# Optimization experiments

Measured on AMD Instinct MI355X. Metric: run time of the kernel, lower is better.

## Reference

```python
import jax, jax.numpy as jnp
import numpy as np
from jax import lax

EPS = 1e-5

def conv2d(x, w, b, pad):
    y = lax.conv_general_dilated(x, w, (1, 1), [(pad, pad), (pad, pad)],
                                 dimension_numbers=('NCHW', 'OIHW', 'NCHW'))
    return y + b[None, :, None, None]

def batchnorm(x, gamma, beta):
    mean = jnp.mean(x, axis=(0, 2, 3), keepdims=True)
    var = jnp.var(x, axis=(0, 2, 3), keepdims=True)  # biased, as torch BN training mode
    return gamma[None, :, None, None] * (x - mean) * lax.rsqrt(var + EPS) + beta[None, :, None, None]

def maxpool2(x):
    return lax.reduce_window(x, -jnp.inf, lax.max, (1, 1, 2, 2), (1, 1, 2, 2), 'VALID')

def upsample(x, s):
    N, C, H, W = x.shape
    return jax.image.resize(x, (N, C, H * s, W * s), method='bilinear')

def select_topvar(x, k=3):
    # per-sample, per-channel unbiased variance; gather top-k variance channels
    N, C, H, W = x.shape
    v = jnp.var(x.reshape(N, C, H * W), axis=-1, ddof=1)  # [N, C]
    _, idx = lax.top_k(v, k)                              # argsort(-v)[:k]
    return jnp.take_along_axis(x, idx[:, :, None, None], axis=1)

def setup_inputs() -> dict:
    key = jax.random.key(0)
    ks = jax.random.split(key, 16)
    n_channel, n_class = 10, 5
    d = {}
    d['x'] = jax.random.normal(ks[0], (16, n_channel, 512, 512), jnp.float32)
    sc = 0.1
    d['w_ext1'] = jax.random.normal(ks[1], (16, n_channel, 1, 1), jnp.float32) * sc
    d['b_ext1'] = jnp.zeros((16,), jnp.float32)
    d['g_ebn1'] = jnp.ones((16,), jnp.float32)
    d['be_ebn1'] = jnp.zeros((16,), jnp.float32)
    d['w_ext2'] = jax.random.normal(ks[2], (16, 16, 1, 1), jnp.float32) * sc
    d['b_ext2'] = jnp.zeros((16,), jnp.float32)
    d['g_ebn2'] = jnp.ones((16,), jnp.float32)
    d['be_ebn2'] = jnp.zeros((16,), jnp.float32)
    d['w_c1'] = jax.random.normal(ks[3], (8, 3, 3, 3), jnp.float32) * sc
    d['b_c1'] = jnp.zeros((8,), jnp.float32)
    d['w_c2'] = jax.random.normal(ks[4], (16, 8, 3, 3), jnp.float32) * sc
    d['b_c2'] = jnp.zeros((16,), jnp.float32)
    d['g_bn1'] = jnp.ones((16,), jnp.float32)
    d['be_bn1'] = jnp.zeros((16,), jnp.float32)
    d['g_bn2'] = jnp.ones((8,), jnp.float32)
    d['be_bn2'] = jnp.zeros((8,), jnp.float32)
    d['w_1k'] = jax.random.normal(ks[5], (n_class, 24, 1, 1), jnp.float32) * sc
    d['b_1k'] = jnp.zeros((n_class,), jnp.float32)
    return d

def reference(x, w_ext1, b_ext1, g_ebn1, be_ebn1, w_ext2, b_ext2, g_ebn2, be_ebn2,
              w_c1, b_c1, w_c2, b_c2, g_bn1, be_bn1, g_bn2, be_bn2, w_1k, b_1k):
    # bandExtract: 1x1 conv -> BN -> sigmoid, twice
    h = jax.nn.sigmoid(batchnorm(conv2d(x, w_ext1, b_ext1, 0), g_ebn1, be_ebn1))
    h = jax.nn.sigmoid(batchnorm(conv2d(h, w_ext2, b_ext2, 0), g_ebn2, be_ebn2))
    # featureSelect: keep 3 channels with largest per-sample variance
    x0 = select_topvar(h, 3)                                   # [N,3,H,W]
    x1 = maxpool2(jax.nn.sigmoid(conv2d(x0, w_c1, b_c1, 1)))   # [N,8,H/2,W/2]
    x2 = maxpool2(jax.nn.sigmoid(conv2d(x1, w_c2, b_c2, 1)))   # [N,16,H/4,W/4]
    x2 = batchnorm(jax.nn.relu(upsample(x2, 4)), g_bn1, be_bn1)  # [N,16,H,W]
    x1 = batchnorm(jax.nn.relu(upsample(x1, 2)), g_bn2, be_bn2)  # [N,8,H,W]
    merge = jnp.concatenate([x1, x2], axis=1)                    # [N,24,H,W]
    return conv2d(merge, w_1k, b_1k, 0)                          # [N,n_class,H,W]
```

## Files before the change

### kernel.cpp

```cpp
#include <hip/hip_runtime.h>
#include <hip/hip_fp16.h>
#include <math.h>

#define N_    16
#define CIN_  10
#define CB_   16
#define H_    512
#define W_    512
#define HW_   (512*512)
#define EPSF  1e-5f

__device__ __forceinline__ float sgm(float z){
  float e = __builtin_amdgcn_exp2f(z * -1.44269504088896f);
  return __builtin_amdgcn_rcpf(1.0f + e);
}

__global__ void k_zero(double* __restrict__ p, int n){
  int i = blockIdx.x*256 + threadIdx.x;
  if (i < n) p[i] = 0.0;
}

template<int NB, int C>
__global__ void k_finp(const double* __restrict__ P, const float* __restrict__ g,
                       const float* __restrict__ be, float* __restrict__ AB, double invM){
  __shared__ double rs[256], rq[256];
  const int t = threadIdx.x;
  const int c = t % C, slot = t / C, nslot = 256 / C;
  const int tot = N_ * NB;
  double s=0.0, q=0.0;
  for (int j = slot; j < tot; j += nslot){
    int n = j / NB, b = j - n*NB;
    size_t idx = ((size_t)((n*C + c)*NB + b))*2;
    s += P[idx]; q += P[idx+1];
  }
  rs[t]=s; rq[t]=q; __syncthreads();
  for (int h = nslot>>1; h>0; h>>=1){
    if (slot < h){ rs[t] += rs[t + h*C]; rq[t] += rq[t + h*C]; }
    __syncthreads();
  }
  if (slot == 0){
    double mean = rs[c]*invM;
    double var  = rq[c]*invM - mean*mean;
    float a = g[c]*rsqrtf((float)var + EPSF);
    AB[c]   = a;
    AB[C+c] = be[c] - (float)mean*a;
  }
}

__global__ void k_fin2(const double* __restrict__ S1, const float* __restrict__ g1,
                       const float* __restrict__ be1, float* __restrict__ A1,
                       const double* __restrict__ S2, const float* __restrict__ g2,
                       const float* __restrict__ be2, float* __restrict__ A2,
                       double invM){
  const double* S = (blockIdx.x==0) ? S1 : S2;
  const float*  g = (blockIdx.x==0) ? g1 : g2;
  const float* be = (blockIdx.x==0) ? be1 : be2;
  float*       AB = (blockIdx.x==0) ? A1 : A2;
  const int     C = (blockIdx.x==0) ? 16 : 8;
  int c = threadIdx.x;
  if (c < C){
    double s=0.0,q=0.0;
    for (int n=0;n<N_;++n){ s+=S[(n*C+c)*2]; q+=S[(n*C+c)*2+1]; }
    double mean = s*invM;
    double var  = q*invM - mean*mean;
    float a = g[c]*rsqrtf((float)var + EPSF);
    AB[c]   = a;
    AB[C+c] = be[c] - (float)mean*a;
  }
}

__global__ __launch_bounds__(256) void k_cov(
    const float* __restrict__ x, double* __restrict__ SP)
{
  const int n = blockIdx.y;
  const int base = blockIdx.x*4096;
  const float* xp = x + (size_t)n*CIN_*HW_;
  float s[CIN_], p[55];
#pragma unroll
  for (int i=0;i<CIN_;++i) s[i]=0.f;
#pragma unroll
  for (int i=0;i<55;++i) p[i]=0.f;
#pragma unroll 1
  for (int it=0; it<4; ++it){
    const int off = base + it*1024 + threadIdx.x*4;
    float4 xv[CIN_];
#pragma unroll
    for (int ci=0; ci<CIN_; ++ci)
      xv[ci] = *(const float4*)(xp + (size_t)ci*HW_ + off);
#pragma unroll
    for (int ci=0; ci<CIN_; ++ci)
      s[ci] += xv[ci].x + xv[ci].y + xv[ci].z + xv[ci].w;
    int k=0;
#pragma unroll
    for (int i=0;i<CIN_;++i)
#pragma unroll
      for (int j=i;j<CIN_;++j,++k)
        p[k] += xv[i].x*xv[j].x + xv[i].y*xv[j].y + xv[i].z*xv[j].z + xv[i].w*xv[j].w;
  }
  __shared__ float red[4][65];
  const int lane = threadIdx.x & 63, wid = threadIdx.x >> 6;
#pragma unroll
  for (int k=0;k<65;++k){
    float v = (k<CIN_) ? s[k] : p[k-CIN_];
    for (int o=32;o>0;o>>=1) v += __shfl_down(v,o);
    if (lane==0) red[wid][k]=v;
  }
  __syncthreads();
  if (threadIdx.x < 65){
    float v = red[0][threadIdx.x]+red[1][threadIdx.x]+red[2][threadIdx.x]+red[3][threadIdx.x];
    atomicAdd(&SP[n*65+threadIdx.x], (double)v);
  }
}

__global__ void k_fin1(const double* __restrict__ SP, const float* __restrict__ w1,
                       const float* __restrict__ b1, const float* __restrict__ g,
                       const float* __restrict__ be, float* __restrict__ AB,
                       float* __restrict__ W1f, float* __restrict__ b1f){
  __shared__ double Sm[CIN_], Cv[55];
  int t = threadIdx.x;
  if (t < 65){
    double s = 0.0;
    for (int n=0;n<N_;++n) s += SP[n*65+t];
    if (t < CIN_) Sm[t] = s; else Cv[t-CIN_] = s;
  }
  __syncthreads();
  if (t < CB_){
    const double M = 16.0*(double)HW_;
    double b = (double)b1[t];
    double wd[CIN_];
    double lin = 0.0;
    for (int i=0;i<CIN_;++i){ wd[i] = (double)w1[t*CIN_+i]; lin += wd[i]*Sm[i]/M; }
    double mean = b + lin;
    double ey2 = b*b + 2.0*b*lin;
    int k=0;
    for (int i=0;i<CIN_;++i)
      for (int j=i;j<CIN_;++j,++k)
        ey2 += (i==j ? 1.0 : 2.0) * wd[i]*wd[j]*(Cv[k]/M);
    double var = ey2 - mean*mean;
    float a = g[t]*rsqrtf((float)var + EPSF);
    float sh = be[t] - (float)mean*a;
    AB[t] = a;
    AB[CB_+t] = sh;
    b1f[t] = a*b1[t] + sh;
    for (int i=0;i<CIN_;++i) W1f[t*CIN_+i] = a*w1[t*CIN_+i];
  }
}

__global__ __launch_bounds__(256) void k_band2(
    const float* __restrict__ x,
    const float* __restrict__ W1f, const float* __restrict__ b1f,
    const float* __restrict__ w2, const float* __restrict__ b2,
    __half* __restrict__ B, double* __restrict__ S2p)
{
  const int n = blockIdx.y;
  const int base = blockIdx.x*4096;
  const float* xp = x + (size_t)n*CIN_*HW_;
  __half* bp = B + (size_t)n*CB_*HW_;
  float sum[CB_], sq[CB_];
#pragma unroll
  for (int c=0;c<CB_;++c){ sum[c]=0.f; sq[c]=0.f; }
#pragma unroll 1
  for (int it=0; it<4; ++it){
    const int p = base + it*1024 + threadIdx.x*4;
    float4 xv[CIN_];
#pragma unroll
    for (int ci=0; ci<CIN_; ++ci)
      xv[ci] = *(const float4*)(xp + (size_t)ci*HW_ + p);
    float4 s[CB_];
#pragma unroll
    for (int co=0; co<CB_; ++co){
      float bb = b1f[co];
      float ox=bb, oy=bb, oz=bb, ow=bb;
#pragma unroll
      for (int ci=0; ci<CIN_; ++ci){
        float w = W1f[co*CIN_+ci];
        ox += w*xv[ci].x; oy += w*xv[ci].y; oz += w*xv[ci].z; ow += w*xv[ci].w;
      }
      s[co].x = sgm(ox); s[co].y = sgm(oy);
      s[co].z = sgm(oz); s[co].w = sgm(ow);
    }
#pragma unroll
    for (int co=0; co<CB_; ++co){
      float bb = b2[co];
      float ox=bb, oy=bb, oz=bb, ow=bb;
#pragma unroll
      for (int ci=0; ci<CB_; ++ci){
        float w = w2[co*CB_+ci];
        ox += w*s[ci].x; oy += w*s[ci].y; oz += w*s[ci].z; ow += w*s[ci].w;
      }
      union { __half2 h[2]; uint2 u; } cu;
      cu.h[0] = __floats2half2_rn(ox, oy);
      cu.h[1] = __floats2half2_rn(oz, ow);
      *(uint2*)(bp + (size_t)co*HW_ + p) = cu.u;
      sum[co] += ox+oy+oz+ow;
      sq[co]  += ox*ox+oy*oy+oz*oz+ow*ow;
    }
  }
  __shared__ float red[4][CB_][2];
  const int lane = threadIdx.x & 63, wid = threadIdx.x >> 6;
#pragma unroll
  for (int c=0;c<CB_;++c){
    float s=sum[c], q=sq[c];
    for (int off=32; off>0; off>>=1){ s += __shfl_down(s,off); q += __shfl_down(q,off); }
    if (lane==0){ red[wid][c][0]=s; red[wid][c][1]=q; }
  }
  __syncthreads();
  if (threadIdx.x < CB_*2){
    int c = threadIdx.x>>1, k = threadIdx.x&1;
    float t = red[0][c][k]+red[1][c][k]+red[2][c][k]+red[3][c][k];
    S2p[(((size_t)n*CB_ + c)*64 + blockIdx.x)*2 + k] = (double)t;
  }
}

__global__ __launch_bounds__(256) void k_varstats(
    const __half* __restrict__ B, const float* __restrict__ AB2, double* __restrict__ SV)
{
  const int n = blockIdx.z, c = blockIdx.y;
  const float a = AB2[c], b = AB2[CB_+c];
  const __half* p = B + ((size_t)(n*CB_+c))*HW_ + blockIdx.x*4096;
  uint2 u0 = *(const uint2*)(p +    0 + threadIdx.x*4);
  uint2 u1 = *(const uint2*)(p + 1024 + threadIdx.x*4);
  uint2 u2 = *(const uint2*)(p + 2048 + threadIdx.x*4);
  uint2 u3 = *(const uint2*)(p + 3072 + threadIdx.x*4);
  float sum=0.f, sq=0.f;
#pragma unroll
  for (int j=0;j<4;++j){
    uint2 uu = (j==0)?u0:((j==1)?u1:((j==2)?u2:u3));
    union { uint2 u; __half2 h[2]; } cu; cu.u = uu;
    float2 f0 = __half22float2(cu.h[0]);
    float2 f1 = __half22float2(cu.h[1]);
    float e0 = sgm(a*f0.x+b), e1 = sgm(a*f0.y+b);
    float e2 = sgm(a*f1.x+b), e3 = sgm(a*f1.y+b);
    sum += e0+e1+e2+e3;
    sq  += e0*e0+e1*e1+e2*e2+e3*e3;
  }
  __shared__ float red[4][2];
  const int lane = threadIdx.x & 63, wid = threadIdx.x >> 6;
  for (int off=32; off>0; off>>=1){ sum += __shfl_down(sum,off); sq += __shfl_down(sq,off); }
  if (lane==0){ red[wid][0]=sum; red[wid][1]=sq; }
  __syncthreads();
  if (threadIdx.x < 2){
    int k = threadIdx.x;
    float t = red[0][k]+red[1][k]+red[2][k]+red[3][k];
    atomicAdd(&SV[(n*CB_+c)*2+k], (double)t);
  }
}

__global__ void k_topk(const double* __restrict__ SV, int* __restrict__ IDX){
  __shared__ double var[N_][CB_];
  int t = threadIdx.x;
  if (t < N_*CB_){
    int n=t>>4, c=t&15;
    double s=SV[t*2], q=SV[t*2+1];
    const double M = (double)HW_;
    var[n][c] = (q - s*s/M)/(M-1.0);
  }
  __syncthreads();
  if (t < N_){
    double v[CB_];
#pragma unroll
    for (int c=0;c<CB_;++c) v[c]=var[t][c];
    for (int k=0;k<3;++k){
      int bi=0; double bv=v[0];
#pragma unroll
      for (int c=1;c<CB_;++c) if (v[c]>bv){ bv=v[c]; bi=c; }
      IDX[t*3+k]=bi; v[bi]=-1e300;
    }
  }
}

__global__ __launch_bounds__(256) void k_conv1p(
    const __half* __restrict__ B, const int* __restrict__ IDX, const float* __restrict__ AB2,
    const float* __restrict__ w, const float* __restrict__ bias,
    float* __restrict__ X1)
{
  const int n = blockIdx.y, ho = blockIdx.x, wo = threadIdx.x;
  __shared__ float tile[3][4][516];
  __shared__ int chs[3];
  __shared__ float ca[3], cb[3];
  if (threadIdx.x < 3){
    int c = IDX[n*3+threadIdx.x];
    chs[threadIdx.x] = c;
    ca[threadIdx.x] = AB2[c];
    cb[threadIdx.x] = AB2[CB_+c];
  }
  __syncthreads();
#pragma unroll
  for (int k=0;k<3;++k){
    const __half* pc = B + ((size_t)(n*CB_+chs[k]))*HW_;
    const float a = ca[k], bb = cb[k];
#pragma unroll
    for (int dy=0;dy<4;++dy){
      const int r = 2*ho-1+dy;
      float tx = 0.f, ty = 0.f;
      if (r>=0 && r<H_){
        const __half2 v = *(const __half2*)(pc + (size_t)r*W_ + 2*wo);
        float2 f = __half22float2(v);
        tx = sgm(a*f.x+bb); ty = sgm(a*f.y+bb);
      }
      tile[k][dy][1+2*wo] = tx;
      tile[k][dy][2+2*wo] = ty;
    }
  }
  if (wo < 24){
    int k = wo>>3, dy = (wo&7)>>1;
    tile[k][dy][(wo&1) ? 513 : 0] = 0.f;
  }
  __syncthreads();
  float in[3][4][4];
#pragma unroll
  for (int k=0;k<3;++k)
#pragma unroll
    for (int dy=0;dy<4;++dy)
#pragma unroll
      for (int dx=0;dx<4;++dx)
        in[k][dy][dx] = tile[k][dy][2*wo+dx];
#pragma unroll
  for (int co=0;co<8;++co){
    float m = -1e30f;
#pragma unroll
    for (int py=0;py<2;++py)
#pragma unroll
    for (int px=0;px<2;++px){
      float acc = bias[co];
#pragma unroll
      for (int k=0;k<3;++k)
#pragma unroll
      for (int kh=0;kh<3;++kh)
#pragma unroll
      for (int kw=0;kw<3;++kw)
        acc += w[((co*3+k)*3+kh)*3+kw] * in[k][py+kh][px+kw];
      m = fmaxf(m, acc);
    }
    X1[((size_t)(n*8+co)*256 + ho)*256 + wo] = sgm(m);
  }
}

__global__ __launch_bounds__(256) void k_conv2p(
    const float* __restrict__ X1, const float* __restrict__ w, const float* __restrict__ bias,
    float* __restrict__ X2)
{
  const int n  = blockIdx.y;
  const int wo = threadIdx.x & 127;
  const int ho = blockIdx.x*2 + (threadIdx.x>>7);
  float acc[16][4];
#pragma unroll
  for (int co=0;co<16;++co){
    float bb = bias[co];
    acc[co][0]=bb; acc[co][1]=bb; acc[co][2]=bb; acc[co][3]=bb;
  }
#pragma unroll 1
  for (int ci=0; ci<8; ++ci){
    const float* p = X1 + ((size_t)(n*8+ci))*65536;
    float patch[4][4];
#pragma unroll
    for (int dy=0;dy<4;++dy){
      int r = 2*ho-1+dy;
      bool rok = (r>=0 && r<256);
#pragma unroll
      for (int dx=0;dx<4;++dx){
        int cc = 2*wo-1+dx;
        patch[dy][dx] = (rok && cc>=0 && cc<256) ? p[r*256+cc] : 0.f;
      }
    }
#pragma unroll
    for (int co=0;co<16;++co){
      const float* wp = w + (co*8+ci)*9;
#pragma unroll
      for (int py=0;py<2;++py)
#pragma unroll
      for (int px=0;px<2;++px){
        float a = acc[co][py*2+px];
#pragma unroll
        for (int kh=0;kh<3;++kh)
#pragma unroll
        for (int kw=0;kw<3;++kw)
          a += wp[kh*3+kw]*patch[py+kh][px+kw];
        acc[co][py*2+px] = a;
      }
    }
  }
#pragma unroll
  for (int co=0;co<16;++co){
    float m = fmaxf(fmaxf(acc[co][0],acc[co][1]), fmaxf(acc[co][2],acc[co][3]));
    X2[((size_t)(n*16+co)*128 + ho)*128 + wo] = sgm(m);
  }
}

__global__ __launch_bounds__(256) void k_upstats(
    const float* __restrict__ X2, const float* __restrict__ X1,
    double* __restrict__ SB1, double* __restrict__ SB2)
{
  const int n = blockIdx.z, y = blockIdx.y;
  const int id = blockIdx.x*256 + threadIdx.x;
  const int ho = id>>7, m = id&127;
  float sum, sq;
  if (y < 16){
    const int c = y;
    const float* p = X2 + ((size_t)(n*16+c))*16384;
    const int q = ho>>2, r = ho&3;
    int rA, rB; float wA;
    if (r==0){ rA=q-1; rB=q;   wA=0.375f; }
    else if (r==1){ rA=q-1; rB=q;   wA=0.125f; }
    else if (r==2){ rA=q;   rB=q+1; wA=0.875f; }
    else          { rA=q;   rB=q+1; wA=0.625f; }
    const float wB = 1.f-wA;
    rA = max(rA,0); rB = min(rB,127);
    const int c0 = max(m-1,0), c1 = m, c2 = min(m+1,127);
    const float* pa = p + rA*128; const float* pb = p + rB*128;
    float t0 = wA*pa[c0]+wB*pb[c0];
    float t1 = wA*pa[c1]+wB*pb[c1];
    float t2 = wA*pa[c2]+wB*pb[c2];
    float o0 = fmaxf(0.375f*t0+0.625f*t1, 0.f);
    float o1 = fmaxf(0.125f*t0+0.875f*t1, 0.f);
    float o2 = fmaxf(0.875f*t1+0.125f*t2, 0.f);
    float o3 = fmaxf(0.625f*t1+0.375f*t2, 0.f);
    sum = o0+o1+o2+o3;
    sq  = o0*o0+o1*o1+o2*o2+o3*o3;
  } else {
    const int c = y-16;
    const float* p = X1 + ((size_t)(n*8+c))*65536;
    const int i = ho>>1, r = ho&1;
    int rA, rB; float wA;
    if (r==0){ rA=i-1; rB=i;   wA=0.25f; }
    else     { rA=i;   rB=i+1; wA=0.75f; }
    const float wB = 1.f-wA;
    rA = max(rA,0); rB = min(rB,255);
    const int c0 = max(2*m-1,0), c1 = 2*m, c2 = 2*m+1, c3 = min(2*m+2,255);
    const float* pa = p + rA*256; const float* pb = p + rB*256;
    float t0 = wA*pa[c0]+wB*pb[c0];
    float t1 = wA*pa[c1]+wB*pb[c1];
    float t2 = wA*pa[c2]+wB*pb[c2];
    float t3 = wA*pa[c3]+wB*pb[c3];
    float o0 = fmaxf(0.25f*t0+0.75f*t1, 0.f);
    float o1 = fmaxf(0.75f*t1+0.25f*t2, 0.f);
    float o2 = fmaxf(0.25f*t1+0.75f*t2, 0.f);
    float o3 = fmaxf(0.75f*t2+0.25f*t3, 0.f);
    sum = o0+o1+o2+o3;
    sq  = o0*o0+o1*o1+o2*o2+o3*o3;
  }
  __shared__ float red[4][2];
  const int lane = threadIdx.x & 63, wid = threadIdx.x >> 6;
  for (int off=32; off>0; off>>=1){ sum += __shfl_down(sum,off); sq += __shfl_down(sq,off); }
  if (lane==0){ red[wid][0]=sum; red[wid][1]=sq; }
  __syncthreads();
  if (threadIdx.x < 2){
    int k = threadIdx.x;
    float t = red[0][k]+red[1][k]+red[2][k]+red[3][k];
    if (y < 16) atomicAdd(&SB1[(n*16+y)*2+k], (double)t);
    else        atomicAdd(&SB2[(n*8+(y-16))*2+k], (double)t);
  }
}

__global__ __launch_bounds__(256) void k_final(
    const float* __restrict__ X1, const float* __restrict__ X2,
    const float* __restrict__ ABB1, const float* __restrict__ ABB2,
    const float* __restrict__ w1k, const float* __restrict__ b1k,
    float* __restrict__ out)
{
  const int n = blockIdx.y, bx = blockIdx.x, tid = threadIdx.x;
  __shared__ float sx1[8][3][256];
  __shared__ float sx2[16][2][128];
  {
    const int R0 = max(bx-1,0), R1 = bx, R2 = min(bx+1,255);
#pragma unroll
    for (int pr=0; pr<24; ++pr){
      const int ch = pr/3, row = pr%3;
      const int rr = (row==0) ? R0 : ((row==1) ? R1 : R2);
      sx1[ch][row][tid] = X1[((size_t)(n*8+ch)*256 + rr)*256 + tid];
    }
  }
  {
    const int q = bx>>1;
    const int Q0 = (bx&1) ? q : max(q-1,0);
    const int Q1 = (bx&1) ? min(q+1,127) : q;
    const int col = tid & 127, half = tid >> 7;
#pragma unroll
    for (int k=0;k<16;++k){
      const int pr = half + 2*k;
      const int ch = pr>>1, row = pr&1;
      const int rr = row ? Q1 : Q0;
      sx2[ch][row][col] = X2[((size_t)(n*16+ch)*128 + rr)*128 + col];
    }
  }
  __syncthreads();

  const int h = 2*bx + (tid>>7);
  const int m = tid & 127;
  float acc[5][4];
#pragma unroll
  for (int cls=0;cls<5;++cls){
    float bb = b1k[cls];
    acc[cls][0]=bb; acc[cls][1]=bb; acc[cls][2]=bb; acc[cls][3]=bb;
  }
  {
    const int r = h&1;
    const float wA = (r==0) ? 0.25f : 0.75f;
    const float wB = 1.f-wA;
    const int paL = r, pbL = r+1;
    const int c0 = max(2*m-1,0), c1 = 2*m, c2 = 2*m+1, c3 = min(2*m+2,255);
#pragma unroll
    for (int c=0;c<8;++c){
      const float* pa = &sx1[c][paL][0];
      const float* pb = &sx1[c][pbL][0];
      float t0 = wA*pa[c0]+wB*pb[c0];
      float t1 = wA*pa[c1]+wB*pb[c1];
      float t2 = wA*pa[c2]+wB*pb[c2];
      float t3 = wA*pa[c3]+wB*pb[c3];
      float o0 = 0.25f*t0+0.75f*t1, o1 = 0.75f*t1+0.25f*t2;
      float o2 = 0.25f*t1+0.75f*t2, o3 = 0.75f*t2+0.25f*t3;
      const float a = ABB2[c], bb = ABB2[8+c];
      o0 = a*fmaxf(o0,0.f)+bb; o1 = a*fmaxf(o1,0.f)+bb;
      o2 = a*fmaxf(o2,0.f)+bb; o3 = a*fmaxf(o3,0.f)+bb;
#pragma unroll
      for (int cls=0;cls<5;++cls){
        float wv = w1k[cls*24+c];
        acc[cls][0]+=wv*o0; acc[cls][1]+=wv*o1; acc[cls][2]+=wv*o2; acc[cls][3]+=wv*o3;
      }
    }
  }
  {
    const int r = h&3;
    float wA;
    if (r==0)      wA=0.375f;
    else if (r==1) wA=0.125f;
    else if (r==2) wA=0.875f;
    else           wA=0.625f;
    const float wB = 1.f-wA;
    const int c0 = max(m-1,0), c1 = m, c2 = min(m+1,127);
#pragma unroll
    for (int c=0;c<16;++c){
      const float* pa = &sx2[c][0][0];
      const float* pb = &sx2[c][1][0];
      float t0 = wA*pa[c0]+wB*pb[c0];
      float t1 = wA*pa[c1]+wB*pb[c1];
      float t2 = wA*pa[c2]+wB*pb[c2];
      float o0 = 0.375f*t0+0.625f*t1;
      float o1 = 0.125f*t0+0.875f*t1;
      float o2 = 0.875f*t1+0.125f*t2;
      float o3 = 0.625f*t1+0.375f*t2;
      const float a = ABB1[c], bb = ABB1[16+c];
      o0 = a*fmaxf(o0,0.f)+bb; o1 = a*fmaxf(o1,0.f)+bb;
      o2 = a*fmaxf(o2,0.f)+bb; o3 = a*fmaxf(o3,0.f)+bb;
#pragma unroll
      for (int cls=0;cls<5;++cls){
        float wv = w1k[cls*24+8+c];
        acc[cls][0]+=wv*o0; acc[cls][1]+=wv*o1; acc[cls][2]+=wv*o2; acc[cls][3]+=wv*o3;
      }
    }
  }
#pragma unroll
  for (int cls=0;cls<5;++cls){
    float4 v; v.x=acc[cls][0]; v.y=acc[cls][1]; v.z=acc[cls][2]; v.w=acc[cls][3];
    *(float4*)(out + ((size_t)(n*5+cls))*HW_ + (size_t)h*W_ + 4*m) = v;
  }
}

extern "C" void kernel_launch(void* const* d_in, const int* in_sizes, int n_in,
                              void* d_out, int out_size, void* d_ws, size_t ws_size,
                              hipStream_t stream) {
  const float* x       = (const float*)d_in[0];
  const float* w_ext1  = (const float*)d_in[1];
  const float* b_ext1  = (const float*)d_in[2];
  const float* g_ebn1  = (const float*)d_in[3];
  const float* be_ebn1 = (const float*)d_in[4];
  const float* w_ext2  = (const float*)d_in[5];
  const float* b_ext2  = (const float*)d_in[6];
  const float* g_ebn2  = (const float*)d_in[7];
  const float* be_ebn2 = (const float*)d_in[8];
  const float* w_c1    = (const float*)d_in[9];
  const float* b_c1    = (const float*)d_in[10];
  const float* w_c2    = (const float*)d_in[11];
  const float* b_c2    = (const float*)d_in[12];
  const float* g_bn1   = (const float*)d_in[13];
  const float* be_bn1  = (const float*)d_in[14];
  const float* g_bn2   = (const float*)d_in[15];
  const float* be_bn2  = (const float*)d_in[16];
  const float* w_1k    = (const float*)d_in[17];
  const float* b_1k    = (const float*)d_in[18];
  float* outp = (float*)d_out;

  char* ws = (char*)d_ws;
  __half* B = (__half*)ws;
  float* X1 = (float*)(ws + 268435456);
  float* X2 = (float*)(ws + 268435456 + 33554432);
  double* S2p = (double*)(ws + 268435456);
  char*  sb = ws + 268435456 + 33554432 + 16777216;
  double* SP  = (double*)sb;
  double* SV  = SP  + 1040;
  double* SB1 = SV  + 512;
  double* SB2 = SB1 + 512;
  float*  AB1  = (float*)(SB2 + 256);
  float*  AB2  = AB1 + 32;
  float*  ABB1 = AB2 + 32;
  float*  ABB2 = ABB1 + 32;
  float*  W1f  = ABB2 + 16;
  float*  b1f  = W1f + 160;
  int*    IDX  = (int*)(b1f + 16);

  const double invM_bn = 1.0/4194304.0;

  k_zero<<<10,256,0,stream>>>(SP, 2320);
  k_cov<<<dim3(64,16),256,0,stream>>>(x, SP);
  k_fin1<<<1,128,0,stream>>>(SP, w_ext1, b_ext1, g_ebn1, be_ebn1, AB1, W1f, b1f);
  k_band2<<<dim3(64,16),256,0,stream>>>(x, W1f, b1f, w_ext2, b_ext2, B, S2p);
  k_finp<64,16><<<1,256,0,stream>>>(S2p, g_ebn2, be_ebn2, AB2, invM_bn);
  k_varstats<<<dim3(64,16,16),256,0,stream>>>(B, AB2, SV);
  k_topk<<<1,256,0,stream>>>(SV, IDX);
  k_conv1p<<<dim3(256,16),256,0,stream>>>(B, IDX, AB2, w_c1, b_c1, X1);
  k_conv2p<<<dim3(64,16),256,0,stream>>>(X1, w_c2, b_c2, X2);
  k_upstats<<<dim3(256,24,16),256,0,stream>>>(X2, X1, SB1, SB2);
  k_fin2<<<2,64,0,stream>>>(SB1, g_bn1, be_bn1, ABB1, SB2, g_bn2, be_bn2, ABB2, invM_bn);
  k_final<<<dim3(256,16),256,0,stream>>>(X1, X2, ABB1, ABB2, w_1k, b_1k, outp);
}
```

Before: 738.8 us.

## Fold tiny finalize kernels into consumers and replace atomics with partial buffers

```diff
diff --git a/kernel.cpp b/kernel.cpp
--- a/kernel.cpp
+++ b/kernel.cpp
@@ -15,63 +15,12 @@
   return __builtin_amdgcn_rcpf(1.0f + e);
 }
 
-__global__ void k_zero(double* __restrict__ p, int n){
-  int i = blockIdx.x*256 + threadIdx.x;
-  if (i < n) p[i] = 0.0;
-}
-
-template<int NB, int C>
-__global__ void k_finp(const double* __restrict__ P, const float* __restrict__ g,
-                       const float* __restrict__ be, float* __restrict__ AB, double invM){
-  __shared__ double rs[256], rq[256];
-  const int t = threadIdx.x;
-  const int c = t % C, slot = t / C, nslot = 256 / C;
-  const int tot = N_ * NB;
-  double s=0.0, q=0.0;
-  for (int j = slot; j < tot; j += nslot){
-    int n = j / NB, b = j - n*NB;
-    size_t idx = ((size_t)((n*C + c)*NB + b))*2;
-    s += P[idx]; q += P[idx+1];
-  }
-  rs[t]=s; rq[t]=q; __syncthreads();
-  for (int h = nslot>>1; h>0; h>>=1){
-    if (slot < h){ rs[t] += rs[t + h*C]; rq[t] += rq[t + h*C]; }
-    __syncthreads();
-  }
-  if (slot == 0){
-    double mean = rs[c]*invM;
-    double var  = rq[c]*invM - mean*mean;
-    float a = g[c]*rsqrtf((float)var + EPSF);
-    AB[c]   = a;
-    AB[C+c] = be[c] - (float)mean*a;
-  }
-}
-
-__global__ void k_fin2(const double* __restrict__ S1, const float* __restrict__ g1,
-                       const float* __restrict__ be1, float* __restrict__ A1,
-                       const double* __restrict__ S2, const float* __restrict__ g2,
-                       const float* __restrict__ be2, float* __restrict__ A2,
-                       double invM){
-  const double* S = (blockIdx.x==0) ? S1 : S2;
-  const float*  g = (blockIdx.x==0) ? g1 : g2;
-  const float* be = (blockIdx.x==0) ? be1 : be2;
-  float*       AB = (blockIdx.x==0) ? A1 : A2;
-  const int     C = (blockIdx.x==0) ? 16 : 8;
-  int c = threadIdx.x;
-  if (c < C){
-    double s=0.0,q=0.0;
-    for (int n=0;n<N_;++n){ s+=S[(n*C+c)*2]; q+=S[(n*C+c)*2+1]; }
-    double mean = s*invM;
-    double var  = q*invM - mean*mean;
-    float a = g[c]*rsqrtf((float)var + EPSF);
-    AB[c]   = a;
-    AB[C+c] = be[c] - (float)mean*a;
-  }
-}
-
 __global__ __launch_bounds__(256) void k_cov(
-    const float* __restrict__ x, double* __restrict__ SP)
+    const float* __restrict__ x, double* __restrict__ SPp, double* __restrict__ SBz)
 {
+  if (blockIdx.x==0 && blockIdx.y==0){
+    for (int i=threadIdx.x; i<768; i+=256) SBz[i]=0.0;
+  }
   const int n = blockIdx.y;
   const int base = blockIdx.x*4096;
   const float* xp = x + (size_t)n*CIN_*HW_;
@@ -108,20 +57,21 @@
   __syncthreads();
   if (threadIdx.x < 65){
     float v = red[0][threadIdx.x]+red[1][threadIdx.x]+red[2][threadIdx.x]+red[3][threadIdx.x];
-    atomicAdd(&SP[n*65+threadIdx.x], (double)v);
-  }
-}
-
-__global__ void k_fin1(const double* __restrict__ SP, const float* __restrict__ w1,
+    SPp[(size_t)threadIdx.x*1024 + (size_t)n*64 + blockIdx.x] = (double)v;
+  }
+}
+
+__global__ void k_fin1(const double* __restrict__ SPp, const float* __restrict__ w1,
                        const float* __restrict__ b1, const float* __restrict__ g,
-                       const float* __restrict__ be, float* __restrict__ AB,
+                       const float* __restrict__ be,
                        float* __restrict__ W1f, float* __restrict__ b1f){
   __shared__ double Sm[CIN_], Cv[55];
-  int t = threadIdx.x;
-  if (t < 65){
+  const int t = threadIdx.x, lane = t & 63, wv = t >> 6;
+  for (int k = wv; k < 65; k += 4){
     double s = 0.0;
-    for (int n=0;n<N_;++n) s += SP[n*65+t];
-    if (t < CIN_) Sm[t] = s; else Cv[t-CIN_] = s;
+    for (int j = 0; j < 16; ++j) s += SPp[(size_t)k*1024 + lane + 64*j];
+    for (int o = 32; o > 0; o >>= 1) s += __shfl_down(s, o);
+    if (lane == 0){ if (k < CIN_) Sm[k] = s; else Cv[k-CIN_] = s; }
   }
   __syncthreads();
   if (t < CB_){
@@ -139,8 +89,6 @@
     double var = ey2 - mean*mean;
     float a = g[t]*rsqrtf((float)var + EPSF);
     float sh = be[t] - (float)mean*a;
-    AB[t] = a;
-    AB[CB_+t] = sh;
     b1f[t] = a*b1[t] + sh;
     for (int i=0;i<CIN_;++i) W1f[t*CIN_+i] = a*w1[t*CIN_+i];
   }
@@ -213,10 +161,34 @@
 }
 
 __global__ __launch_bounds__(256) void k_varstats(
-    const __half* __restrict__ B, const float* __restrict__ AB2, double* __restrict__ SV)
+    const __half* __restrict__ B, const double* __restrict__ S2p,
+    const float* __restrict__ g2, const float* __restrict__ be2,
+    double* __restrict__ SVp)
 {
   const int n = blockIdx.z, c = blockIdx.y;
-  const float a = AB2[c], b = AB2[CB_+c];
+  __shared__ double rs[256], rq[256];
+  __shared__ float sab[2];
+  {
+    double s=0.0, q=0.0;
+    for (int e = threadIdx.x; e < 1024; e += 256){
+      int nn = e >> 6, bb = e & 63;
+      size_t idx = (((size_t)nn*CB_ + c)*64 + bb)*2;
+      s += S2p[idx]; q += S2p[idx+1];
+    }
+    rs[threadIdx.x]=s; rq[threadIdx.x]=q; __syncthreads();
+    for (int h=128; h>0; h>>=1){
+      if (threadIdx.x < h){ rs[threadIdx.x]+=rs[threadIdx.x+h]; rq[threadIdx.x]+=rq[threadIdx.x+h]; }
+      __syncthreads();
+    }
+    if (threadIdx.x==0){
+      const double invM = 1.0/4194304.0;
+      double mean = rs[0]*invM, var = rq[0]*invM - mean*mean;
+      float a = g2[c]*rsqrtf((float)var + EPSF);
+      sab[0]=a; sab[1]=be2[c] - (float)mean*a;
+    }
+    __syncthreads();
+  }
+  const float a = sab[0], b = sab[1];
   const __half* p = B + ((size_t)(n*CB_+c))*HW_ + blockIdx.x*4096;
   uint2 u0 = *(const uint2*)(p +    0 + threadIdx.x*4);
   uint2 u1 = *(const uint2*)(p + 1024 + threadIdx.x*4);
@@ -242,49 +214,74 @@
   if (threadIdx.x < 2){
     int k = threadIdx.x;
     float t = red[0][k]+red[1][k]+red[2][k]+red[3][k];
-    atomicAdd(&SV[(n*CB_+c)*2+k], (double)t);
-  }
-}
-
-__global__ void k_topk(const double* __restrict__ SV, int* __restrict__ IDX){
-  __shared__ double var[N_][CB_];
-  int t = threadIdx.x;
-  if (t < N_*CB_){
-    int n=t>>4, c=t&15;
-    double s=SV[t*2], q=SV[t*2+1];
-    const double M = (double)HW_;
-    var[n][c] = (q - s*s/M)/(M-1.0);
-  }
-  __syncthreads();
-  if (t < N_){
-    double v[CB_];
-#pragma unroll
-    for (int c=0;c<CB_;++c) v[c]=var[t][c];
-    for (int k=0;k<3;++k){
-      int bi=0; double bv=v[0];
-#pragma unroll
-      for (int c=1;c<CB_;++c) if (v[c]>bv){ bv=v[c]; bi=c; }
-      IDX[t*3+k]=bi; v[bi]=-1e300;
-    }
+    SVp[(((size_t)n*CB_ + c)*64 + blockIdx.x)*2 + k] = (double)t;
   }
 }
 
 __global__ __launch_bounds__(256) void k_conv1p(
-    const __half* __restrict__ B, const int* __restrict__ IDX, const float* __restrict__ AB2,
+    const __half* __restrict__ B, const double* __restrict__ SVp,
+    const double* __restrict__ S2p, const float* __restrict__ g2,
+    const float* __restrict__ be2,
     const float* __restrict__ w, const float* __restrict__ bias,
     float* __restrict__ X1)
 {
   const int n = blockIdx.y, ho = blockIdx.x, wo = threadIdx.x;
-  __shared__ float tile[3][4][516];
+  __shared__ double rs[256], rq[256];
+  __shared__ double var[CB_];
   __shared__ int chs[3];
   __shared__ float ca[3], cb[3];
-  if (threadIdx.x < 3){
-    int c = IDX[n*3+threadIdx.x];
-    chs[threadIdx.x] = c;
-    ca[threadIdx.x] = AB2[c];
-    cb[threadIdx.x] = AB2[CB_+c];
-  }
-  __syncthreads();
+  {
+    int c = threadIdx.x >> 4, slot = threadIdx.x & 15;
+    double s=0.0, q=0.0;
+    for (int j=0;j<4;++j){
+      int bb = slot*4 + j;
+      size_t idx = (((size_t)n*CB_ + c)*64 + bb)*2;
+      s += SVp[idx]; q += SVp[idx+1];
+    }
+    rs[threadIdx.x]=s; rq[threadIdx.x]=q; __syncthreads();
+    for (int h=8; h>0; h>>=1){
+      if (slot < h){ rs[threadIdx.x]+=rs[threadIdx.x+h]; rq[threadIdx.x]+=rq[threadIdx.x+h]; }
+      __syncthreads();
+    }
+    if (slot==0){
+      double s_=rs[threadIdx.x], q_=rq[threadIdx.x];
+      const double M = (double)HW_;
+      var[c] = (q_ - s_*s_/M)/(M-1.0);
+    }
+    __syncthreads();
+    if (threadIdx.x==0){
+      double v[CB_];
+      for (int c2=0;c2<CB_;++c2) v[c2]=var[c2];
+      for (int k=0;k<3;++k){
+        int bi=0; double bv=v[0];
+        for (int c2=1;c2<CB_;++c2) if (v[c2]>bv){ bv=v[c2]; bi=c2; }
+        chs[k]=bi; v[bi]=-1e300;
+      }
+    }
+    __syncthreads();
+    for (int k3=0;k3<3;++k3){
+      int c2 = chs[k3];
+      double s2=0.0, q2=0.0;
+      for (int e = threadIdx.x; e < 1024; e += 256){
+        int nn = e >> 6, bb = e & 63;
+        size_t idx = (((size_t)nn*CB_ + c2)*64 + bb)*2;
+        s2 += S2p[idx]; q2 += S2p[idx+1];
+      }
+      rs[threadIdx.x]=s2; rq[threadIdx.x]=q2; __syncthreads();
+      for (int h=128; h>0; h>>=1){
+        if (threadIdx.x < h){ rs[threadIdx.x]+=rs[threadIdx.x+h]; rq[threadIdx.x]+=rq[threadIdx.x+h]; }
+        __syncthreads();
+      }
+      if (threadIdx.x==0){
+        const double invM = 1.0/4194304.0;
+        double mean = rs[0]*invM, vv = rq[0]*invM - mean*mean;
+        float a = g2[c2]*rsqrtf((float)vv + EPSF);
+        ca[k3]=a; cb[k3]=be2[c2] - (float)mean*a;
+      }
+      __syncthreads();
+    }
+  }
+  __shared__ float tile[3][4][516];
 #pragma unroll
   for (int k=0;k<3;++k){
     const __half* pc = B + ((size_t)(n*CB_+chs[k]))*HW_;
@@ -454,11 +451,31 @@
 
 __global__ __launch_bounds__(256) void k_final(
     const float* __restrict__ X1, const float* __restrict__ X2,
-    const float* __restrict__ ABB1, const float* __restrict__ ABB2,
+    const double* __restrict__ SB1, const double* __restrict__ SB2,
+    const float* __restrict__ g1, const float* __restrict__ be1,
+    const float* __restrict__ g2, const float* __restrict__ be2,
     const float* __restrict__ w1k, const float* __restrict__ b1k,
     float* __restrict__ out)
 {
   const int n = blockIdx.y, bx = blockIdx.x, tid = threadIdx.x;
+  __shared__ float sA1[32];
+  __shared__ float sA2[16];
+  if (tid < 16){
+    double s=0.0,q=0.0;
+    for (int nn=0;nn<N_;++nn){ s+=SB1[(nn*16+tid)*2]; q+=SB1[(nn*16+tid)*2+1]; }
+    const double invM = 1.0/4194304.0;
+    double mean=s*invM, vv=q*invM-mean*mean;
+    float a=g1[tid]*rsqrtf((float)vv+EPSF);
+    sA1[tid]=a; sA1[16+tid]=be1[tid]-(float)mean*a;
+  } else if (tid < 24){
+    int c = tid-16;
+    double s=0.0,q=0.0;
+    for (int nn=0;nn<N_;++nn){ s+=SB2[(nn*8+c)*2]; q+=SB2[(nn*8+c)*2+1]; }
+    const double invM = 1.0/4194304.0;
+    double mean=s*invM, vv=q*invM-mean*mean;
+    float a=g2[c]*rsqrtf((float)vv+EPSF);
+    sA2[c]=a; sA2[8+c]=be2[c]-(float)mean*a;
+  }
   __shared__ float sx1[8][3][256];
   __shared__ float sx2[16][2][128];
   {
@@ -509,7 +526,7 @@
       float t3 = wA*pa[c3]+wB*pb[c3];
       float o0 = 0.25f*t0+0.75f*t1, o1 = 0.75f*t1+0.25f*t2;
       float o2 = 0.25f*t1+0.75f*t2, o3 = 0.75f*t2+0.25f*t3;
-      const float a = ABB2[c], bb = ABB2[8+c];
+      const float a = sA2[c], bb = sA2[8+c];
       o0 = a*fmaxf(o0,0.f)+bb; o1 = a*fmaxf(o1,0.f)+bb;
       o2 = a*fmaxf(o2,0.f)+bb; o3 = a*fmaxf(o3,0.f)+bb;
 #pragma unroll
@@ -539,7 +556,7 @@
       float o1 = 0.125f*t0+0.875f*t1;
       float o2 = 0.875f*t1+0.125f*t2;
       float o3 = 0.625f*t1+0.375f*t2;
-      const float a = ABB1[c], bb = ABB1[16+c];
+      const float a = sA1[c], bb = sA1[16+c];
       o0 = a*fmaxf(o0,0.f)+bb; o1 = a*fmaxf(o1,0.f)+bb;
       o2 = a*fmaxf(o2,0.f)+bb; o3 = a*fmaxf(o3,0.f)+bb;
 #pragma unroll
@@ -582,34 +599,23 @@
 
   char* ws = (char*)d_ws;
   __half* B = (__half*)ws;
+  double* S2p = (double*)(ws + 134217728);
+  double* SVp = (double*)(ws + 134217728 + 262144);
+  double* SPp = (double*)(ws + 134217728 + 524288);
   float* X1 = (float*)(ws + 268435456);
   float* X2 = (float*)(ws + 268435456 + 33554432);
-  double* S2p = (double*)(ws + 268435456);
   char*  sb = ws + 268435456 + 33554432 + 16777216;
-  double* SP  = (double*)sb;
-  double* SV  = SP  + 1040;
-  double* SB1 = SV  + 512;
+  double* SB1 = (double*)sb;
   double* SB2 = SB1 + 512;
-  float*  AB1  = (float*)(SB2 + 256);
-  float*  AB2  = AB1 + 32;
-  float*  ABB1 = AB2 + 32;
-  float*  ABB2 = ABB1 + 32;
-  float*  W1f  = ABB2 + 16;
-  float*  b1f  = W1f + 160;
-  int*    IDX  = (int*)(b1f + 16);
-
-  const double invM_bn = 1.0/4194304.0;
-
-  k_zero<<<10,256,0,stream>>>(SP, 2320);
-  k_cov<<<dim3(64,16),256,0,stream>>>(x, SP);
-  k_fin1<<<1,128,0,stream>>>(SP, w_ext1, b_ext1, g_ebn1, be_ebn1, AB1, W1f, b1f);
+  float*  W1f = (float*)(SB2 + 256);
+  float*  b1f = W1f + 160;
+
+  k_cov<<<dim3(64,16),256,0,stream>>>(x, SPp, SB1);
+  k_fin1<<<1,256,0,stream>>>(SPp, w_ext1, b_ext1, g_ebn1, be_ebn1, W1f, b1f);
   k_band2<<<dim3(64,16),256,0,stream>>>(x, W1f, b1f, w_ext2, b_ext2, B, S2p);
-  k_finp<64,16><<<1,256,0,stream>>>(S2p, g_ebn2, be_ebn2, AB2, invM_bn);
-  k_varstats<<<dim3(64,16,16),256,0,stream>>>(B, AB2, SV);
-  k_topk<<<1,256,0,stream>>>(SV, IDX);
-  k_conv1p<<<dim3(256,16),256,0,stream>>>(B, IDX, AB2, w_c1, b_c1, X1);
+  k_varstats<<<dim3(64,16,16),256,0,stream>>>(B, S2p, g_ebn2, be_ebn2, SVp);
+  k_conv1p<<<dim3(256,16),256,0,stream>>>(B, SVp, S2p, g_ebn2, be_ebn2, w_c1, b_c1, X1);
   k_conv2p<<<dim3(64,16),256,0,stream>>>(X1, w_c2, b_c2, X2);
   k_upstats<<<dim3(256,24,16),256,0,stream>>>(X2, X1, SB1, SB2);
-  k_fin2<<<2,64,0,stream>>>(SB1, g_bn1, be_bn1, ABB1, SB2, g_bn2, be_bn2, ABB2, invM_bn);
-  k_final<<<dim3(256,16),256,0,stream>>>(X1, X2, ABB1, ABB2, w_1k, b_1k, outp);
-}
+  k_final<<<dim3(256,16),256,0,stream>>>(X1, X2, SB1, SB2, g_bn1, be_bn1, g_bn2, be_bn2, w_1k, b_1k, outp);
+}
```

Measured after the change: 883.4 us. 19.6% more time.
